# Kernel optimization log

Hardware: AMD Instinct MI355X
Metric: run time of the kernel (lower is better)

The kernel has to match this reference:

```python
import jax, jax.numpy as jnp
import numpy as np

EMB = 384
HID = 256
HEADS = 4
HD = HID // HEADS  # 64
LAYERS = 2
M_DOCS = 32
TOTAL = 4096  # 1 query + 32 docs + 4063 sentences
LN_EPS = 1e-5


def _layernorm(x, scale, bias):
    mu = jnp.mean(x, axis=-1, keepdims=True)
    var = jnp.mean(jnp.square(x - mu), axis=-1, keepdims=True)
    return (x - mu) * jax.lax.rsqrt(var + LN_EPS) * scale + bias


def setup_inputs() -> dict:
    key = jax.random.key(0)
    ks = jax.random.split(key, 12)
    g = 0.05  # small init scale (stand-in for xavier)
    return {
        "node_embeddings": jax.random.normal(ks[0], (TOTAL, EMB), jnp.float32),
        "adj": jax.random.randint(ks[1], (TOTAL, TOTAL), 0, 2, jnp.int32),
        "num_docs": M_DOCS,
        "proj_w": jax.random.normal(ks[2], (HID, EMB), jnp.float32) * g,
        "proj_b": jnp.zeros((HID,), jnp.float32),
        "ln_scale": jnp.ones((LAYERS, HID), jnp.float32),
        "ln_bias": jnp.zeros((LAYERS, HID), jnp.float32),
        "gat_W": jax.random.normal(ks[3], (LAYERS, HEADS, HD, HID), jnp.float32) * g,
        "gat_a": jax.random.normal(ks[4], (LAYERS, HEADS, 2 * HD), jnp.float32) * g,
        "fusion_w": jax.random.normal(ks[5], (HID, 2 * HID + 2), jnp.float32) * g,
        "fusion_b": jnp.zeros((HID,), jnp.float32),
        "out_w": jax.random.normal(ks[6], (HID,), jnp.float32) * g,
        "out_b": jnp.float32(0.5),
    }


def reference(node_embeddings, adj, num_docs, proj_w, proj_b, ln_scale, ln_bias,
              gat_W, gat_a, fusion_w, fusion_b, out_w, out_b):
    T = node_embeddings.shape[0]
    M = num_docs
    N = T - 1 - M  # number of sentences
    # input projection + relu (dropout = identity in eval)
    h = jax.nn.relu(node_embeddings @ proj_w.T + proj_b)  # (T, HID)
    # query-guided sentence re-weighting
    q = h[0:1]                     # (1, HID)
    s = h[1 + M:]                  # (N, HID)
    qn = q / (jnp.linalg.norm(q, axis=1, keepdims=True) + 1e-8)
    sn = s / (jnp.linalg.norm(s, axis=1, keepdims=True) + 1e-8)
    cos = (qn @ sn.T).reshape(-1, 1)          # (N,1)
    s = s + 0.8 * q * cos
    h = jnp.concatenate([h[:1 + M], s], axis=0)
    mask = (adj == 0)[None]                   # (1,T,T)
    for i in range(LAYERS):
        res = h
        x = _layernorm(h, ln_scale[i], ln_bias[i])
        Wh = jnp.einsum('nd,hkd->hnk', x, gat_W[i])                # (H,T,HD)
        # concat-attention a.[Wh_i ; Wh_j] == a_src.Wh_i + a_dst.Wh_j
        src = jnp.einsum('hnk,hk->hn', Wh, gat_a[i, :, :HD])       # (H,T)
        dst = jnp.einsum('hnk,hk->hn', Wh, gat_a[i, :, HD:])       # (H,T)
        e = jax.nn.leaky_relu(src[:, :, None] + dst[:, None, :], 0.2)  # (H,T,T)
        e = jnp.where(mask, -jnp.inf, e)
        attn = jax.nn.softmax(e, axis=-1)                          # softmax over j
        hn = jnp.einsum('hij,hjk->hik', attn, Wh)                  # (H,T,HD)
        hcat = jnp.transpose(hn, (1, 0, 2)).reshape(T, HEADS * HD)
        h = 0.5 * jax.nn.relu(hcat) + 0.5 * res
    qh = h[0:1]
    sh = h[1 + M:]
    scores = (qh @ sh.T) / (HID ** 0.5)       # (1,N)
    aw = jax.nn.softmax(scores, axis=-1)
    awT = aw.T                                # (N,1)
    qw = qh * (awT + 0.5)                     # (N,HID)
    qnf = qh / (jnp.linalg.norm(qh, axis=1, keepdims=True) + 1e-8)
    snf = sh / (jnp.linalg.norm(sh, axis=1, keepdims=True) + 1e-8)
    cosf = (qnf @ snf.T).reshape(-1, 1)       # (N,1)
    feat = jnp.concatenate([sh, qw, cosf, awT], axis=1)  # (N, 2*HID+2)
    g = jax.nn.relu(feat @ fusion_w.T + fusion_b)
    out = g @ out_w + out_b                   # (N,)
    return out + 0.5 * cosf[:, 0]
```

## Files before the change

### kernel.cpp

```cpp
#include <hip/hip_runtime.h>
#include <hip/hip_bf16.h>
#include <stdint.h>

#define TOTAL 4096
#define EMB 384
#define MD 32
#define NDOCS (TOTAL - 1 - MD)
#define LN_EPS 1e-5f
#define NEGF (-1e30f)

typedef __hip_bfloat16 bf16;
typedef unsigned short ushort_t;
typedef __attribute__((ext_vector_type(8))) short short8;
typedef __attribute__((ext_vector_type(4))) float f32x4;
typedef __attribute__((ext_vector_type(2))) float f32x2;

__device__ __forceinline__ float ldf(const void* p, int i, int isbf) {
    return isbf ? __bfloat162float(((const bf16*)p)[i]) : ((const float*)p)[i];
}

__device__ __forceinline__ unsigned f2bf(float x) {
    return (__float_as_uint(x) + 0x8000u) >> 16;
}

__device__ __forceinline__ unsigned fenc(float f) {
    unsigned u = __float_as_uint(f);
    return (u >> 31) ? ~u : (u | 0x80000000u);
}
__device__ __forceinline__ float fdec(unsigned k) {
    return __uint_as_float((k & 0x80000000u) ? (k & 0x7FFFFFFFu) : ~k);
}

#define TRTOT (EMB * 256 + 2 * 65536 + 514 * 256)
__global__ __launch_bounds__(256) void k_adjmask(
        const int* adj, unsigned long long* maskb,
        const uint16_t* embp, int* flag, unsigned* dmaxu,
        const void* proj_w, const void* proj_b, const void* gat_W,
        const void* fusion_w,
        float* projT, float* gatT, float* fwT, float* qrow) {
    __shared__ int red[4];
    __shared__ float qred2[4];
    __shared__ float embs[EMB];
    int bid = blockIdx.x, t = threadIdx.x;
    int w = t >> 6, l = t & 63;
    int cnt = 0;
    for (int k = t; k < 4096; k += 256) {
        uint16_t wd = embp[2 * k];
        int e = (wd >> 7) & 0xFF;
        if (e >= 100 && e <= 140) cnt++;
    }
    for (int o = 32; o > 0; o >>= 1) cnt += __shfl_down(cnt, o);
    if ((t & 63) == 0) red[t >> 6] = cnt;
    __syncthreads();
    int isbf = (red[0] + red[1] + red[2] + red[3] > 2048) ? 1 : 0;
    if (bid == 0 && t == 0) flag[0] = isbf;
    if (bid < 4096) {
        const int4* adj4 = (const int4*)(adj + (size_t)bid * TOTAL);
        unsigned long long parts[4];
#pragma unroll
        for (int it = 0; it < 4; it++) {
            int4 a = adj4[it * 256 + t];
            unsigned nib = (a.x != 0 ? 1u : 0u) | (a.y != 0 ? 2u : 0u) |
                           (a.z != 0 ? 4u : 0u) | (a.w != 0 ? 8u : 0u);
            parts[it] = (unsigned long long)nib << (4 * (l & 15));
        }
#pragma unroll
        for (int it = 0; it < 4; it++) {
            unsigned long long m = parts[it];
            m |= __shfl_xor(m, 1);
            m |= __shfl_xor(m, 2);
            m |= __shfl_xor(m, 4);
            m |= __shfl_xor(m, 8);
            if ((l & 15) == 0)
                maskb[bid * 64 + it * 16 + w * 4 + (l >> 4)] = m;
        }
        if (bid == 0) {
            for (int idx = t; idx < 2048; idx += 256) dmaxu[idx] = 0x007FFFFFu;
        }
        int idx = bid * 256 + t;
        if (idx < EMB * 256) {
            int c = idx / EMB, d = idx - c * EMB;
            projT[(d >> 2) * 1024 + c * 4 + (d & 3)] = ldf(proj_w, idx, isbf);
        } else if (idx < EMB * 256 + 2 * 65536) {
            int r = idx - EMB * 256;
            int ll = r >> 16, rem = r & 65535;
            int c = rem >> 8, d = rem & 255;
            gatT[ll * 65536 + (d >> 2) * 1024 + c * 4 + (d & 3)] = ldf(gat_W, r, isbf);
        } else if (idx < TRTOT) {
            int r = idx - (EMB * 256 + 2 * 65536);
            int c = r / 514, j = r - c * 514;
            fwT[(j >> 2) * 1024 + c * 4 + (j & 3)] = ldf(fusion_w, r, isbf);
        }
    } else {
        for (int d = t; d < EMB; d += 256) embs[d] = ldf((const void*)embp, d, isbf);
        __syncthreads();
        float p0 = 0.f, p1 = 0.f, p2 = 0.f, p3 = 0.f;
        if (!isbf) {
            const float4* W4 = (const float4*)proj_w;
#pragma unroll 8
            for (int k = 0; k < 96; k++) {
                float4 wv = W4[t * 96 + k];
                float4 e = *(const float4*)&embs[k * 4];
                p0 = fmaf(e.x, wv.x, p0); p1 = fmaf(e.y, wv.y, p1);
                p2 = fmaf(e.z, wv.z, p2); p3 = fmaf(e.w, wv.w, p3);
            }
        } else {
            const uint4* W4 = (const uint4*)proj_w;
#pragma unroll 8
            for (int k = 0; k < 48; k++) {
                uint4 raw = W4[t * 48 + k];
                unsigned rws[4] = {raw.x, raw.y, raw.z, raw.w};
#pragma unroll
                for (int q = 0; q < 4; q++) {
                    float we = __uint_as_float(rws[q] << 16);
                    float wo = __uint_as_float(rws[q] & 0xFFFF0000u);
                    if ((q & 1) == 0) {
                        p0 = fmaf(embs[k * 8 + 2 * q], we, p0);
                        p1 = fmaf(embs[k * 8 + 2 * q + 1], wo, p1);
                    } else {
                        p2 = fmaf(embs[k * 8 + 2 * q], we, p2);
                        p3 = fmaf(embs[k * 8 + 2 * q + 1], wo, p3);
                    }
                }
            }
        }
        float accq = (p0 + p2) + (p1 + p3);
        float qv = fmaxf(accq + ldf(proj_b, t, isbf), 0.f);
        qrow[t] = qv;
        float a = qv * qv;
        for (int o = 32; o > 0; o >>= 1) a += __shfl_down(a, o);
        if ((t & 63) == 0) qred2[t >> 6] = a;
        __syncthreads();
        if (t == 0) qrow[256] = sqrtf(qred2[0] + qred2[1] + qred2[2] + qred2[3]) + 1e-8f;
    }
}

#define LR 8
__global__ __launch_bounds__(512) void k_lnwh(
        const void* emb, const void* proj_b, const float* projT,
        float* h, const float* gatT, const void* ln_scale, const void* ln_bias,
        const void* gat_a, ushort_t* whswz, float* srcb, unsigned* d12g,
        unsigned* dmaxu, int layer, const int* flagp, const float* qrow) {
    __shared__ float embs[8][EMB];
    __shared__ float xs[8][256];
    __shared__ float xpart[8][4][256];
    int isbf = flagp[0];
    int t5 = threadIdx.x;
    int w8 = t5 >> 6;
    int l = t5 & 63;
    int i0 = blockIdx.x * LR;
    int myrow = i0 + w8;
    float hv[4];
    if (layer == 0) {
        for (int idx = t5; idx < 8 * EMB; idx += 512) {
            int r = idx / EMB, d = idx % EMB;
            embs[r][d] = ldf(emb, (i0 + r) * EMB + d, isbf);
        }
        __syncthreads();
        const float4* pT4 = (const float4*)projT;
        float ap[8][4];
#pragma unroll
        for (int r = 0; r < 8; r++)
#pragma unroll
            for (int cc = 0; cc < 4; cc++) ap[r][cc] = 0.f;
        for (int s = 0; s < 12; s++) {
            int k4 = w8 * 12 + s;
            float4 wv[4];
#pragma unroll
            for (int cc = 0; cc < 4; cc++) wv[cc] = pT4[k4 * 256 + cc * 64 + l];
#pragma unroll
            for (int r = 0; r < 8; r++) {
                float4 x = *(const float4*)&embs[r][k4 * 4];
#pragma unroll
                for (int cc = 0; cc < 4; cc++) {
                    ap[r][cc] = fmaf(x.x, wv[cc].x, ap[r][cc]);
                    ap[r][cc] = fmaf(x.y, wv[cc].y, ap[r][cc]);
                    ap[r][cc] = fmaf(x.z, wv[cc].z, ap[r][cc]);
                    ap[r][cc] = fmaf(x.w, wv[cc].w, ap[r][cc]);
                }
            }
        }
#pragma unroll
        for (int r = 0; r < 4; r++)
#pragma unroll
            for (int cc = 0; cc < 4; cc++) xpart[w8][r][cc * 64 + l] = ap[r][cc];
        __syncthreads();
        float bias[4];
#pragma unroll
        for (int cc = 0; cc < 4; cc++) bias[cc] = ldf(proj_b, cc * 64 + l, isbf);
        if (w8 < 4) {
#pragma unroll
            for (int cc = 0; cc < 4; cc++) {
                float s = 0.f;
#pragma unroll
                for (int g = 0; g < 8; g++) s += xpart[g][w8][cc * 64 + l];
                hv[cc] = fmaxf(s + bias[cc], 0.f);
            }
        }
        __syncthreads();
#pragma unroll
        for (int r = 4; r < 8; r++)
#pragma unroll
            for (int cc = 0; cc < 4; cc++) xpart[w8][r - 4][cc * 64 + l] = ap[r][cc];
        __syncthreads();
        if (w8 >= 4) {
#pragma unroll
            for (int cc = 0; cc < 4; cc++) {
                float s = 0.f;
#pragma unroll
                for (int g = 0; g < 8; g++) s += xpart[g][w8 - 4][cc * 64 + l];
                hv[cc] = fmaxf(s + bias[cc], 0.f);
            }
        }
        if (myrow >= 1 + MD) {
            float qv[4];
#pragma unroll
            for (int cc = 0; cc < 4; cc++) qv[cc] = qrow[cc * 64 + l];
            float b = 0.f, c = 0.f;
#pragma unroll
            for (int cc = 0; cc < 4; cc++) {
                b = fmaf(hv[cc], hv[cc], b);
                c = fmaf(qv[cc], hv[cc], c);
            }
            for (int o = 32; o > 0; o >>= 1) { b += __shfl_xor(b, o); c += __shfl_xor(c, o); }
            float qn = qrow[256];
            float k = 0.8f * (c / (qn * (sqrtf(b) + 1e-8f)));
#pragma unroll
            for (int cc = 0; cc < 4; cc++) hv[cc] += k * qv[cc];
        }
#pragma unroll
        for (int cc = 0; cc < 4; cc++) h[(size_t)myrow * 256 + cc * 64 + l] = hv[cc];
    } else {
#pragma unroll
        for (int cc = 0; cc < 4; cc++) hv[cc] = h[(size_t)myrow * 256 + cc * 64 + l];
    }
    {
        float a = 0.f, b2 = 0.f;
#pragma unroll
        for (int cc = 0; cc < 4; cc++) { a += hv[cc]; b2 = fmaf(hv[cc], hv[cc], b2); }
        for (int o = 32; o > 0; o >>= 1) { a += __shfl_xor(a, o); b2 += __shfl_xor(b2, o); }
        float mu = a * (1.f / 256.f);
        float var = b2 * (1.f / 256.f) - mu * mu;
        float rs = rsqrtf(var + LN_EPS);
#pragma unroll
        for (int cc = 0; cc < 4; cc++) {
            float sc = ldf(ln_scale, layer * 256 + cc * 64 + l, isbf);
            float lb = ldf(ln_bias, layer * 256 + cc * 64 + l, isbf);
            xs[w8][cc * 64 + l] = (hv[cc] - mu) * rs * sc + lb;
        }
    }
    __syncthreads();
    const float4* gT4 = (const float4*)(gatT + layer * 65536);
    float aw[8][4];
#pragma unroll
    for (int r = 0; r < 8; r++)
#pragma unroll
        for (int cc = 0; cc < 4; cc++) aw[r][cc] = 0.f;
    for (int s = 0; s < 8; s++) {
        int k4 = w8 * 8 + s;
        float4 wv[4];
#pragma unroll
        for (int cc = 0; cc < 4; cc++) wv[cc] = gT4[k4 * 256 + cc * 64 + l];
#pragma unroll
        for (int r = 0; r < 8; r++) {
            float4 x = *(const float4*)&xs[r][k4 * 4];
#pragma unroll
            for (int cc = 0; cc < 4; cc++) {
                aw[r][cc] = fmaf(x.x, wv[cc].x, aw[r][cc]);
                aw[r][cc] = fmaf(x.y, wv[cc].y, aw[r][cc]);
                aw[r][cc] = fmaf(x.z, wv[cc].z, aw[r][cc]);
                aw[r][cc] = fmaf(x.w, wv[cc].w, aw[r][cc]);
            }
        }
    }
#pragma unroll
    for (int r = 0; r < 4; r++)
#pragma unroll
        for (int cc = 0; cc < 4; cc++) xpart[w8][r][cc * 64 + l] = aw[r][cc];
    __syncthreads();
    float acc2[4];
    if (w8 < 4) {
#pragma unroll
        for (int cc = 0; cc < 4; cc++) {
            float s = 0.f;
#pragma unroll
            for (int g = 0; g < 8; g++) s += xpart[g][w8][cc * 64 + l];
            acc2[cc] = s;
        }
    }
    __syncthreads();
#pragma unroll
    for (int r = 4; r < 8; r++)
#pragma unroll
        for (int cc = 0; cc < 4; cc++) xpart[w8][r - 4][cc * 64 + l] = aw[r][cc];
    __syncthreads();
    if (w8 >= 4) {
#pragma unroll
        for (int cc = 0; cc < 4; cc++) {
            float s = 0.f;
#pragma unroll
            for (int g = 0; g < 8; g++) s += xpart[g][w8 - 4][cc * 64 + l];
            acc2[cc] = s;
        }
    }
#pragma unroll
    for (int cc = 0; cc < 4; cc++) {
        int col = cc * 64 + l;
        int off = (myrow >> 6) * 16384 + (col >> 6) * 4096 + ((myrow >> 3) & 7) * 512 +
                  ((col >> 4) & 3) * 128 + (col & 15) * 8 + (myrow & 7);
        whswz[off] = (ushort_t)f2bf(acc2[cc]);
    }
    float sv[4], dv[4];
#pragma unroll
    for (int cc = 0; cc < 4; cc++) {
        float av1 = ldf(gat_a, layer * 512 + cc * 128 + l, isbf);
        float av2 = ldf(gat_a, layer * 512 + cc * 128 + 64 + l, isbf);
        sv[cc] = acc2[cc] * av1;
        dv[cc] = acc2[cc] * av2;
    }
    for (int o = 32; o > 0; o >>= 1) {
#pragma unroll
        for (int cc = 0; cc < 4; cc++) {
            sv[cc] += __shfl_down(sv[cc], o);
            dv[cc] += __shfl_down(dv[cc], o);
        }
    }
    if (l == 0) {
        const float LOG2E = 1.44269504f;
#pragma unroll
        for (int cc = 0; cc < 4; cc++) {
            srcb[cc * 4096 + myrow] = sv[cc];
            float D1 = exp2f(dv[cc] * LOG2E), D2 = exp2f(0.2f * dv[cc] * LOG2E);
            d12g[cc * 4096 + myrow] = (f2bf(D2) << 16) | f2bf(D1);
            atomicMax(&dmaxu[(blockIdx.x & 63) * 16 + cc], fenc(dv[cc]));
        }
    }
}

#define TI 16
__global__ __launch_bounds__(512) void k_pv(const ushort_t* whswz, const float* srcb,
                                            const unsigned* dmaxu, const unsigned* d12g,
                                            const unsigned long long* maskb, float* h) {
    __shared__ unsigned long long mbs[16 * 66];
    __shared__ __align__(16) f32x4 accsh[16 * 64];
    __shared__ __align__(16) float lsh[4][4][4];
    __shared__ float srcs[64];
    __shared__ float dmx[4];
    __shared__ unsigned mlut[4];
    int t = threadIdx.x;
    int W = t >> 6, lane = t & 63;
    int hH = W & 3, kq = W >> 2;
    int quad = lane >> 4, c16 = lane & 15;
    int i0 = blockIdx.x * TI;
    if (t < 4) mlut[t] = (t & 1 ? 0x0000FFFFu : 0u) | (t & 2 ? 0xFFFF0000u : 0u);
    if (t < 256) {
        int hh = t >> 6, sl = t & 63;
        float v = fdec(dmaxu[sl * 16 + hh]);
        for (int o = 32; o > 0; o >>= 1) v = fmaxf(v, __shfl_xor(v, o));
        if (sl == 0) dmx[hh] = v;
    }
    for (int idx = t; idx < 16 * 64; idx += 512) {
        int r = idx >> 6, wd = idx & 63;
        mbs[r * 66 + wd] = maskb[(size_t)(i0 + r) * 64 + wd];
    }
    if (t < 64) srcs[t] = srcb[(t >> 4) * 4096 + i0 + (t & 15)];
    __syncthreads();
    const float LOG2E = 1.44269504f;
    float dm = dmx[hH];
    float src = srcs[hH * 16 + c16];
    float sd = src + dm;
    float rce = -fmaxf(sd, 0.2f * sd);
    float E1 = exp2f((src + rce) * LOG2E);
    float E2 = exp2f((0.2f * src + rce) * LOG2E);
    f32x4 acc[4];
    f32x4 accl = (f32x4){0.f, 0.f, 0.f, 0.f};
#pragma unroll
    for (int ct = 0; ct < 4; ct++) acc[ct] = (f32x4){0.f, 0.f, 0.f, 0.f};
    uint4 onesu;
    unsigned os = (c16 == 0) ? 0x3F803F80u : 0u;
    onesu.x = os; onesu.y = os; onesu.z = os; onesu.w = os;
    short8 bfones = __builtin_bit_cast(short8, onesu);
    const uint4* g4 = (const uint4*)whswz;
    const uint4* d4 = (const uint4*)d12g;
    size_t b0 = (size_t)hH * 512 + (size_t)(kq * 4 + quad) * 64 + c16;
    int dbase = hH * 1024, d0i = kq * 8 + quad * 2;
    uint4 bA0 = g4[b0],        bA1 = g4[b0 + 16],        bA2 = g4[b0 + 32],        bA3 = g4[b0 + 48];
    uint4 bB0 = g4[b0 + 2048], bB1 = g4[b0 + 2048 + 16], bB2 = g4[b0 + 2048 + 32], bB3 = g4[b0 + 2048 + 48];
    uint4 dA0 = d4[dbase + d0i],      dA1 = d4[dbase + d0i + 1];
    uint4 dB0 = d4[dbase + 16 + d0i], dB1 = d4[dbase + 16 + d0i + 1];
    auto pvstep = [&](uint4& B0, uint4& B1, uint4& B2, uint4& B3,
                      uint4& DD0, uint4& DD1, int s) {
        uint4 bc0 = B0, bc1 = B1, bc2 = B2, bc3 = B3;
        uint4 dc0 = DD0, dc1 = DD1;
        if (s < 62) {
            size_t bs = b0 + (size_t)(s + 2) * 2048;
            B0 = g4[bs]; B1 = g4[bs + 16]; B2 = g4[bs + 32]; B3 = g4[bs + 48];
            int di = dbase + (s + 2) * 16 + d0i;
            DD0 = d4[di]; DD1 = d4[di + 1];
        }
        unsigned mby = (unsigned)(mbs[c16 * 66 + s] >> (kq * 32 + quad * 8)) & 0xFFu;
        unsigned dw[8] = {dc0.x, dc0.y, dc0.z, dc0.w, dc1.x, dc1.y, dc1.z, dc1.w};
        unsigned pu[4];
#pragma unroll
        for (int q = 0; q < 4; q++) {
            unsigned a = dw[2 * q], b = dw[2 * q + 1];
            f32x2 D1 = (f32x2){__uint_as_float(a << 16), __uint_as_float(b << 16)};
            f32x2 D2 = (f32x2){__uint_as_float(a & 0xFFFF0000u), __uint_as_float(b & 0xFFFF0000u)};
            f32x2 v1 = D1 * E1;
            f32x2 v2 = D2 * E2;
            f32x2 m = __builtin_elementwise_max(v1, v2);
            unsigned v = ((__float_as_uint(m.x) + 0x8000u) >> 16) |
                         ((__float_as_uint(m.y) + 0x8000u) & 0xFFFF0000u);
            pu[q] = v & mlut[(mby >> (2 * q)) & 3u];
        }
        uint4 afu;
        afu.x = pu[0]; afu.y = pu[1]; afu.z = pu[2]; afu.w = pu[3];
        short8 af = __builtin_bit_cast(short8, afu);
        acc[0] = __builtin_amdgcn_mfma_f32_16x16x32_bf16(af, __builtin_bit_cast(short8, bc0), acc[0], 0, 0, 0);
        acc[1] = __builtin_amdgcn_mfma_f32_16x16x32_bf16(af, __builtin_bit_cast(short8, bc1), acc[1], 0, 0, 0);
        acc[2] = __builtin_amdgcn_mfma_f32_16x16x32_bf16(af, __builtin_bit_cast(short8, bc2), acc[2], 0, 0, 0);
        acc[3] = __builtin_amdgcn_mfma_f32_16x16x32_bf16(af, __builtin_bit_cast(short8, bc3), acc[3], 0, 0, 0);
        accl = __builtin_amdgcn_mfma_f32_16x16x32_bf16(af, bfones, accl, 0, 0, 0);
    };
    for (int sp = 0; sp < 32; sp++) {
        pvstep(bA0, bA1, bA2, bA3, dA0, dA1, 2 * sp);
        pvstep(bB0, bB1, bB2, bB3, dB0, dB1, 2 * sp + 1);
    }
    __syncthreads();
    if (kq == 1) {
#pragma unroll
        for (int ct = 0; ct < 4; ct++)
            accsh[(hH * 4 + ct) * 64 + lane] = acc[ct];
        if (c16 == 0) *(f32x4*)&lsh[hH][quad][0] = accl;
    }
    __syncthreads();
    if (kq == 0) {
        float ls[4];
#pragma unroll
        for (int rr = 0; rr < 4; rr++)
            ls[rr] = __shfl(accl[rr], quad * 16) + lsh[hH][quad][rr];
#pragma unroll
        for (int ct = 0; ct < 4; ct++) {
            f32x4 o = acc[ct] + accsh[(hH * 4 + ct) * 64 + lane];
#pragma unroll
            for (int rr = 0; rr < 4; rr++) {
                int row = i0 + quad * 4 + rr;
                size_t idx = (size_t)row * 256 + hH * 64 + ct * 16 + c16;
                float hn = 0.5f * fmaxf(o[rr] / ls[rr], 0.f) + 0.5f * h[idx];
                h[idx] = hn;
            }
        }
    }
}

__global__ __launch_bounds__(256) void k_scores(const float* h, float* scoresv, float* cosv,
                                                float* swp) {
    int t = threadIdx.x, W = t >> 6, lane = t & 63;
    const float4* h4 = (const float4*)h;
    int gw = blockIdx.x * 4 + W;
    float4 q4 = h4[lane];
    float a = q4.x * q4.x + q4.y * q4.y + q4.z * q4.z + q4.w * q4.w;
    for (int o = 32; o > 0; o >>= 1) a += __shfl_xor(a, o);
    float qn = sqrtf(a) + 1e-8f;
    float mw = NEGF, sw = 0.f;
    for (int n = gw; n < NDOCS; n += 1024) {
        float4 s4 = h4[(size_t)(1 + MD + n) * 64 + lane];
        float b = s4.x * s4.x + s4.y * s4.y + s4.z * s4.z + s4.w * s4.w;
        float c = q4.x * s4.x + q4.y * s4.y + q4.z * s4.z + q4.w * s4.w;
        for (int o = 32; o > 0; o >>= 1) { b += __shfl_xor(b, o); c += __shfl_xor(c, o); }
        float sc = c * (1.f / 16.f);
        if (lane == 0) {
            scoresv[n] = sc;
            cosv[n] = c / (qn * (sqrtf(b) + 1e-8f));
        }
        float mn = fmaxf(mw, sc);
        sw = sw * __expf(mw - mn) + __expf(sc - mn);
        mw = mn;
    }
    if (lane == 0) { swp[2 * gw] = mw; swp[2 * gw + 1] = sw; }
}

#define TN 8
__global__ __launch_bounds__(256) void k_fusion(const float* h,
                                                const float* scoresv, const float* swp,
                                                const float* cosv,
                                                const float* fwT, const void* fusion_b,
                                                const void* out_w, const void* out_bp,
                                                void* outv, const int* flagp) {
    __shared__ float feats2[514][TN];
    __shared__ float qhs[256];
    __shared__ float red[TN][4];
    __shared__ float reds[2][4];
    __shared__ float aws[TN];
    int isbf = flagp[0];
    int t = threadIdx.x;
    int n0 = blockIdx.x * TN;
    qhs[t] = h[t];
    float M = NEGF, S = 0.f;
    for (int idx = t; idx < 1024; idx += 256) {
        float pm = swp[2 * idx], ps = swp[2 * idx + 1];
        float mn = fmaxf(M, pm);
        S = S * __expf(M - mn) + ps * __expf(pm - mn);
        M = mn;
    }
    for (int o = 32; o > 0; o >>= 1) {
        float m2 = __shfl_xor(M, o), s2 = __shfl_xor(S, o);
        float mn = fmaxf(M, m2);
        S = S * __expf(M - mn) + s2 * __expf(m2 - mn);
        M = mn;
    }
    if ((t & 63) == 0) { reds[0][t >> 6] = M; reds[1][t >> 6] = S; }
    __syncthreads();
    float Mf = fmaxf(fmaxf(reds[0][0], reds[0][1]), fmaxf(reds[0][2], reds[0][3]));
    float Sf = reds[1][0] * __expf(reds[0][0] - Mf) + reds[1][1] * __expf(reds[0][1] - Mf) +
               reds[1][2] * __expf(reds[0][2] - Mf) + reds[1][3] * __expf(reds[0][3] - Mf);
    float invS = 1.f / Sf;
    if (t < TN) {
        int n = n0 + t;
        aws[t] = (n < NDOCS) ? __expf(scoresv[n] - Mf) * invS : 0.f;
    }
    __syncthreads();
    for (int idx = t; idx < 514 * TN; idx += 256) {
        int j = idx >> 3, r = idx & 7;
        int n = n0 + r;
        float v = 0.f;
        if (n < NDOCS) {
            if (j < 256) v = h[(size_t)(1 + MD + n) * 256 + j];
            else if (j < 512) v = qhs[j - 256] * (aws[r] + 0.5f);
            else if (j == 512) v = cosv[n];
            else v = aws[r];
        }
        feats2[j][r] = v;
    }
    __syncthreads();
    float acc[TN];
    float bk = ldf(fusion_b, t, isbf);
#pragma unroll
    for (int r = 0; r < TN; r++) acc[r] = bk;
    const float4* fT4 = (const float4*)fwT;
    for (int j0 = 0; j0 < 512; j0 += 8) {
        float4 wa = fT4[(j0 >> 2) * 256 + t];
        float4 wb = fT4[((j0 >> 2) + 1) * 256 + t];
        float wv[8] = {wa.x, wa.y, wa.z, wa.w, wb.x, wb.y, wb.z, wb.w};
#pragma unroll
        for (int u = 0; u < 8; u++) {
            float4 fa = *(const float4*)&feats2[j0 + u][0];
            float4 fb = *(const float4*)&feats2[j0 + u][4];
            acc[0] = fmaf(fa.x, wv[u], acc[0]); acc[1] = fmaf(fa.y, wv[u], acc[1]);
            acc[2] = fmaf(fa.z, wv[u], acc[2]); acc[3] = fmaf(fa.w, wv[u], acc[3]);
            acc[4] = fmaf(fb.x, wv[u], acc[4]); acc[5] = fmaf(fb.y, wv[u], acc[5]);
            acc[6] = fmaf(fb.z, wv[u], acc[6]); acc[7] = fmaf(fb.w, wv[u], acc[7]);
        }
    }
    {
        float4 wt = fT4[128 * 256 + t];
#pragma unroll
        for (int r = 0; r < TN; r++) acc[r] = fmaf(feats2[512][r], wt.x, acc[r]);
#pragma unroll
        for (int r = 0; r < TN; r++) acc[r] = fmaf(feats2[513][r], wt.y, acc[r]);
    }
    float ow = ldf(out_w, t, isbf);
    float outb = ldf(out_bp, 0, isbf);
#pragma unroll
    for (int r = 0; r < TN; r++) {
        float o = fmaxf(acc[r], 0.f) * ow;
        for (int off = 32; off > 0; off >>= 1) o += __shfl_down(o, off);
        if ((t & 63) == 0) red[r][t >> 6] = o;
    }
    __syncthreads();
    if (t < TN) {
        int n = n0 + t;
        if (n < NDOCS) {
            float o = red[t][0] + red[t][1] + red[t][2] + red[t][3] + outb + 0.5f * cosv[n];
            if (isbf) ((bf16*)outv)[n] = __float2bfloat16(o);
            else      ((float*)outv)[n] = o;
        }
    }
}

extern "C" void kernel_launch(void* const* d_in, const int* in_sizes, int n_in,
                              void* d_out, int out_size, void* d_ws, size_t ws_size,
                              hipStream_t stream) {
    const void* emb      = d_in[0];
    const int*  adj      = (const int*)d_in[1];
    const void* proj_w   = d_in[3];
    const void* proj_b   = d_in[4];
    const void* ln_scale = d_in[5];
    const void* ln_bias  = d_in[6];
    const void* gat_W    = d_in[7];
    const void* gat_a    = d_in[8];
    const void* fusion_w = d_in[9];
    const void* fusion_b = d_in[10];
    const void* out_w    = d_in[11];
    const void* out_b    = d_in[12];

    unsigned long long* maskb = (unsigned long long*)d_ws;
    int* flag = (int*)((char*)d_ws + (size_t)4096 * 64 * 8);
    float* f = (float*)((char*)d_ws + (size_t)4096 * 64 * 8 + 256);
    float* h       = f; f += 4096 * 256;
    float* srcb    = f; f += 4 * 4096;
    unsigned* d12g = (unsigned*)f; f += 4 * 4096;
    unsigned* dmaxu = (unsigned*)f; f += 2048;
    float* projT   = f; f += EMB * 256;
    float* gatT    = f; f += 2 * 65536;
    float* fwT     = f; f += 129 * 1024;
    float* scoresv = f; f += 4096;
    float* cosv    = f; f += 4096;
    float* swpart  = f; f += 2048;
    float* qrowb   = f; f += 260;
    ushort_t* whswz = (ushort_t*)f; f += 4096 * 256 / 2;

    k_adjmask<<<dim3(4097), dim3(256), 0, stream>>>(adj, maskb, (const uint16_t*)emb, flag,
                                                    dmaxu, proj_w, proj_b, gat_W, fusion_w,
                                                    projT, gatT, fwT, qrowb);
    for (int layer = 0; layer < 2; layer++) {
        k_lnwh<<<dim3(TOTAL / LR), dim3(512), 0, stream>>>(emb, proj_b, projT, h, gatT,
                                                           ln_scale, ln_bias, gat_a,
                                                           whswz, srcb, d12g,
                                                           dmaxu + layer * 1024, layer, flag,
                                                           qrowb);
        k_pv<<<dim3(TOTAL / TI), dim3(512), 0, stream>>>(whswz, srcb, dmaxu + layer * 1024,
                                                         d12g, maskb, h);
    }
    k_scores<<<dim3(256), dim3(256), 0, stream>>>(h, scoresv, cosv, swpart);
    k_fusion<<<dim3((NDOCS + TN - 1) / TN), dim3(256), 0, stream>>>(h, scoresv, swpart,
                                                                    cosv, fwT, fusion_b, out_w,
                                                                    out_b, (void*)d_out, flag);
}
```

Measured before the change: 317.0 us.

## Split attention key dimension across two blocks with atomic last-block combine

The PV attention kernel now launches a second grid dimension that splits the 4096 key columns in half. Each block writes its partial numerator and row-sum to a global scratch buffer, and a per-tile atomic counter picks the last-arriving block to merge both halves and apply the residual update. The aim is to double the number of blocks (256 to 512) so the GPU is better filled and each block's serial loop is halved. The cost is extra global traffic for the partials plus fence and atomic synchronisation.

After: 376.9 us. 18.9% more time.

```diff
diff --git a/kernel.cpp b/kernel.cpp
--- a/kernel.cpp
+++ b/kernel.cpp
@@ -37,7 +37,7 @@
         const uint16_t* embp, int* flag, unsigned* dmaxu,
         const void* proj_w, const void* proj_b, const void* gat_W,
         const void* fusion_w,
-        float* projT, float* gatT, float* fwT, float* qrow) {
+        float* projT, float* gatT, float* fwT, float* qrow, unsigned* pvflag) {
     __shared__ int red[4];
     __shared__ float qred2[4];
     __shared__ float embs[EMB];
@@ -76,6 +76,7 @@
         }
         if (bid == 0) {
             for (int idx = t; idx < 2048; idx += 256) dmaxu[idx] = 0x007FFFFFu;
+            for (int idx = t; idx < 512; idx += 256) pvflag[idx] = 0u;
         }
         int idx = bid * 256 + t;
         if (idx < EMB * 256) {
@@ -340,18 +341,21 @@
 #define TI 16
 __global__ __launch_bounds__(512) void k_pv(const ushort_t* whswz, const float* srcb,
                                             const unsigned* dmaxu, const unsigned* d12g,
-                                            const unsigned long long* maskb, float* h) {
-    __shared__ unsigned long long mbs[16 * 66];
+                                            const unsigned long long* maskb, float* h,
+                                            f32x4* pvp, f32x4* lpartb, unsigned* pvflag) {
+    __shared__ unsigned long long mbs[16 * 34];
     __shared__ __align__(16) f32x4 accsh[16 * 64];
     __shared__ __align__(16) float lsh[4][4][4];
     __shared__ float srcs[64];
     __shared__ float dmx[4];
     __shared__ unsigned mlut[4];
+    __shared__ int ordsh;
     int t = threadIdx.x;
     int W = t >> 6, lane = t & 63;
     int hH = W & 3, kq = W >> 2;
     int quad = lane >> 4, c16 = lane & 15;
     int i0 = blockIdx.x * TI;
+    int by = blockIdx.y;
     if (t < 4) mlut[t] = (t & 1 ? 0x0000FFFFu : 0u) | (t & 2 ? 0xFFFF0000u : 0u);
     if (t < 256) {
         int hh = t >> 6, sl = t & 63;
@@ -359,9 +363,9 @@
         for (int o = 32; o > 0; o >>= 1) v = fmaxf(v, __shfl_xor(v, o));
         if (sl == 0) dmx[hh] = v;
     }
-    for (int idx = t; idx < 16 * 64; idx += 512) {
-        int r = idx >> 6, wd = idx & 63;
-        mbs[r * 66 + wd] = maskb[(size_t)(i0 + r) * 64 + wd];
+    for (int idx = t; idx < 16 * 32; idx += 512) {
+        int r = idx >> 5, wd = idx & 31;
+        mbs[r * 34 + wd] = maskb[(size_t)(i0 + r) * 64 + by * 32 + wd];
     }
     if (t < 64) srcs[t] = srcb[(t >> 4) * 4096 + i0 + (t & 15)];
     __syncthreads();
@@ -382,8 +386,8 @@
     short8 bfones = __builtin_bit_cast(short8, onesu);
     const uint4* g4 = (const uint4*)whswz;
     const uint4* d4 = (const uint4*)d12g;
-    size_t b0 = (size_t)hH * 512 + (size_t)(kq * 4 + quad) * 64 + c16;
-    int dbase = hH * 1024, d0i = kq * 8 + quad * 2;
+    size_t b0 = (size_t)by * 65536 + hH * 512 + (size_t)(kq * 4 + quad) * 64 + c16;
+    int dbase = hH * 1024 + by * 512, d0i = kq * 8 + quad * 2;
     uint4 bA0 = g4[b0],        bA1 = g4[b0 + 16],        bA2 = g4[b0 + 32],        bA3 = g4[b0 + 48];
     uint4 bB0 = g4[b0 + 2048], bB1 = g4[b0 + 2048 + 16], bB2 = g4[b0 + 2048 + 32], bB3 = g4[b0 + 2048 + 48];
     uint4 dA0 = d4[dbase + d0i],      dA1 = d4[dbase + d0i + 1];
@@ -392,13 +396,13 @@
                       uint4& DD0, uint4& DD1, int s) {
         uint4 bc0 = B0, bc1 = B1, bc2 = B2, bc3 = B3;
         uint4 dc0 = DD0, dc1 = DD1;
-        if (s < 62) {
+        if (s < 30) {
             size_t bs = b0 + (size_t)(s + 2) * 2048;
             B0 = g4[bs]; B1 = g4[bs + 16]; B2 = g4[bs + 32]; B3 = g4[bs + 48];
             int di = dbase + (s + 2) * 16 + d0i;
             DD0 = d4[di]; DD1 = d4[di + 1];
         }
-        unsigned mby = (unsigned)(mbs[c16 * 66 + s] >> (kq * 32 + quad * 8)) & 0xFFu;
+        unsigned mby = (unsigned)(mbs[c16 * 34 + s] >> (kq * 32 + quad * 8)) & 0xFFu;
         unsigned dw[8] = {dc0.x, dc0.y, dc0.z, dc0.w, dc1.x, dc1.y, dc1.z, dc1.w};
         unsigned pu[4];
 #pragma unroll
@@ -422,7 +426,7 @@
         acc[3] = __builtin_amdgcn_mfma_f32_16x16x32_bf16(af, __builtin_bit_cast(short8, bc3), acc[3], 0, 0, 0);
         accl = __builtin_amdgcn_mfma_f32_16x16x32_bf16(af, bfones, accl, 0, 0, 0);
     };
-    for (int sp = 0; sp < 32; sp++) {
+    for (int sp = 0; sp < 16; sp++) {
         pvstep(bA0, bA1, bA2, bA3, dA0, dA1, 2 * sp);
         pvstep(bB0, bB1, bB2, bB3, dB0, dB1, 2 * sp + 1);
     }
@@ -434,19 +438,44 @@
         if (c16 == 0) *(f32x4*)&lsh[hH][quad][0] = accl;
     }
     __syncthreads();
+    f32x4 o[4];
     if (kq == 0) {
+        size_t slot = (((size_t)blockIdx.x * 4 + hH) * 2 + by);
+        f32x4* op = pvp + slot * 256 + (size_t)lane * 4;
+#pragma unroll
+        for (int ct = 0; ct < 4; ct++) {
+            o[ct] = acc[ct] + accsh[(hH * 4 + ct) * 64 + lane];
+            op[ct] = o[ct];
+        }
+        if (c16 == 0) {
+            f32x4 lvv = accl + *(const f32x4*)&lsh[hH][quad][0];
+            lpartb[slot * 4 + quad] = lvv;
+        }
+    }
+    __syncthreads();
+    if (t == 0) {
+        __threadfence();
+        ordsh = (int)atomicAdd(&pvflag[blockIdx.x], 1u);
+        __threadfence();
+    }
+    __syncthreads();
+    if (ordsh == 0) return;
+    if (kq == 0) {
+        size_t oslot = (((size_t)blockIdx.x * 4 + hH) * 2 + (1 - by));
+        const f32x4* tp = pvp + oslot * 256 + (size_t)lane * 4;
+        f32x4 lvt = lpartb[oslot * 4 + quad];
         float ls[4];
 #pragma unroll
         for (int rr = 0; rr < 4; rr++)
-            ls[rr] = __shfl(accl[rr], quad * 16) + lsh[hH][quad][rr];
+            ls[rr] = (__shfl(accl[rr], quad * 16) + lsh[hH][quad][rr]) + lvt[rr];
 #pragma unroll
         for (int ct = 0; ct < 4; ct++) {
-            f32x4 o = acc[ct] + accsh[(hH * 4 + ct) * 64 + lane];
+            f32x4 ot = o[ct] + tp[ct];
 #pragma unroll
             for (int rr = 0; rr < 4; rr++) {
                 int row = i0 + quad * 4 + rr;
                 size_t idx = (size_t)row * 256 + hH * 64 + ct * 16 + c16;
-                float hn = 0.5f * fmaxf(o[rr] / ls[rr], 0.f) + 0.5f * h[idx];
+                float hn = 0.5f * fmaxf(ot[rr] / ls[rr], 0.f) + 0.5f * h[idx];
                 h[idx] = hn;
             }
         }
@@ -608,19 +637,23 @@
     float* cosv    = f; f += 4096;
     float* swpart  = f; f += 2048;
     float* qrowb   = f; f += 260;
+    float* pvpf    = f; f += 2097152;
+    float* lpartf  = f; f += 32768;
+    unsigned* pvflag = (unsigned*)f; f += 512;
     ushort_t* whswz = (ushort_t*)f; f += 4096 * 256 / 2;
 
     k_adjmask<<<dim3(4097), dim3(256), 0, stream>>>(adj, maskb, (const uint16_t*)emb, flag,
                                                     dmaxu, proj_w, proj_b, gat_W, fusion_w,
-                                                    projT, gatT, fwT, qrowb);
+                                                    projT, gatT, fwT, qrowb, pvflag);
     for (int layer = 0; layer < 2; layer++) {
         k_lnwh<<<dim3(TOTAL / LR), dim3(512), 0, stream>>>(emb, proj_b, projT, h, gatT,
                                                            ln_scale, ln_bias, gat_a,
                                                            whswz, srcb, d12g,
                                                            dmaxu + layer * 1024, layer, flag,
                                                            qrowb);
-        k_pv<<<dim3(TOTAL / TI), dim3(512), 0, stream>>>(whswz, srcb, dmaxu + layer * 1024,
-                                                         d12g, maskb, h);
+        k_pv<<<dim3(TOTAL / TI, 2), dim3(512), 0, stream>>>(whswz, srcb, dmaxu + layer * 1024,
+                                                            d12g, maskb, h, (f32x4*)pvpf,
+                                                            (f32x4*)lpartf, pvflag + layer * 256);
     }
     k_scores<<<dim3(256), dim3(256), 0, stream>>>(h, scoresv, cosv, swpart);
     k_fusion<<<dim3((NDOCS + TN - 1) / TN), dim3(256), 0, stream>>>(h, scoresv, swpart,
```
